# Optimization experiments

Measured on AMD Instinct MI355X. Metric: run time of the kernel, lower is better.

## Reference

```python
import jax, jax.numpy as jnp
import numpy as np

N = 50000      # nodes
E = 800000     # edges
HID = 64       # hidden_dim
HEADS = 4
DH = HID // HEADS
PIN = 128      # person_in_dim
DIN = 64       # disease_in_dim
NEXP = 4       # num_experts
K = 2          # topk
L = 2          # n_layers
NEG = 0.2      # gat_neg_slope


def setup_inputs() -> dict:
    key = jax.random.key(0)
    ks = iter(jax.random.split(key, 64))
    nrm = lambda shp, s=0.05: jax.random.normal(next(ks), shp, jnp.float32) * s
    d = {}
    d["features"] = jax.random.normal(next(ks), (N, PIN), jnp.float32)
    d["node_types"] = jax.random.randint(next(ks), (N,), 0, 2)
    d["src"] = jax.random.randint(next(ks), (E,), 0, N)
    d["dst"] = jax.random.randint(next(ks), (E,), 0, N)
    d["W_person"] = nrm((PIN, HID)); d["b_person"] = jnp.zeros((HID,), jnp.float32)
    d["W_disease"] = nrm((DIN, HID)); d["b_disease"] = jnp.zeros((HID,), jnp.float32)
    d["gat_W"] = nrm((L, HID, HID)); d["gat_al"] = nrm((L, HEADS, DH)); d["gat_ar"] = nrm((L, HEADS, DH))
    d["gin_eps"] = jnp.zeros((L,), jnp.float32)
    d["gin_W1"] = nrm((L, HID, HID)); d["gin_b1"] = jnp.zeros((L, HID), jnp.float32)
    d["gin_W2"] = nrm((L, HID, HID)); d["gin_b2"] = jnp.zeros((L, HID), jnp.float32)
    for p in ("gat", "gin"):
        d[p + "_gW"] = nrm((HID, NEXP)); d[p + "_gb"] = jnp.zeros((NEXP,), jnp.float32)
        d[p + "_eW1"] = nrm((NEXP, HID, HID // 2)); d[p + "_eb1"] = jnp.zeros((NEXP, HID // 2), jnp.float32)
        d[p + "_eW2"] = nrm((NEXP, HID // 2, HID)); d[p + "_eb2"] = jnp.zeros((NEXP, HID), jnp.float32)
    d["fg_W1"] = nrm((2 * HID, HID)); d["fg_b1"] = jnp.zeros((HID,), jnp.float32)
    d["fg_W2"] = nrm((HID, HID)); d["fg_b2"] = jnp.zeros((HID,), jnp.float32)
    return d


def _edge_softmax(logits, dst):
    m = jax.ops.segment_max(logits, dst, num_segments=N)
    e = jnp.exp(logits - m[dst])
    s = jax.ops.segment_sum(e, dst, num_segments=N)
    return e / (s[dst] + 1e-9)


def _gat(h, src, dst, gat_W, gat_al, gat_ar):
    for l in range(L):
        hW = (h @ gat_W[l]).reshape(N, HEADS, DH)
        el = (hW * gat_al[l]).sum(-1)                    # [N, HEADS]
        er = (hW * gat_ar[l]).sum(-1)
        lg = jax.nn.leaky_relu(el[src] + er[dst], NEG)   # [E, HEADS]
        a = _edge_softmax(lg, dst)
        out = jax.ops.segment_sum(hW[src] * a[:, :, None], dst, num_segments=N)
        h2 = out.reshape(N, HID) + h                     # residual=True
        h = jax.nn.relu(h2) if l < L - 1 else h2
    return h


def _gin(h, src, dst, gin_eps, gin_W1, gin_b1, gin_W2, gin_b2):
    deg = jax.ops.segment_sum(jnp.ones((E,), jnp.float32), dst, num_segments=N)
    inv = 1.0 / jnp.maximum(deg, 1.0)
    for l in range(L):
        agg = jax.ops.segment_sum(h[src], dst, num_segments=N) * inv[:, None]  # 'mean' aggregator
        x = (1.0 + gin_eps[l]) * h + agg                 # learn_eps=True
        x = jax.nn.relu(x @ gin_W1[l] + gin_b1[l]) @ gin_W2[l] + gin_b2[l]     # 2-layer MLP
        h = jax.nn.relu(x) if l < L - 1 else x
    return h


def _expert(h, gW, gb, eW1, eb1, eW2, eb2):
    probs = jax.nn.softmax(h @ gW + gb, axis=-1)         # [N, NEXP]
    topv, topi = jax.lax.top_k(probs, K)
    topv = topv / topv.sum(-1, keepdims=True)
    hot = jax.nn.one_hot(topi, NEXP, dtype=h.dtype)      # [N, K, NEXP]
    w = (hot * topv[..., None]).sum(1)                   # [N, NEXP] sparse weights
    e1 = jax.nn.relu(jnp.einsum('nd,edh->neh', h, eW1) + eb1)
    e2 = jnp.einsum('neh,ehd->ned', e1, eW2) + eb2       # [N, NEXP, HID]
    out = (e2 * w[:, :, None]).sum(1)
    f = hot.sum(1).mean(0)                               # routed fraction per expert
    P = probs.mean(0)
    aux = NEXP * jnp.sum(f * P)                          # switch-style load balancing
    return out, aux


def reference(features, node_types, src, dst, W_person, b_person, W_disease, b_disease,
              gat_W, gat_al, gat_ar, gin_eps, gin_W1, gin_b1, gin_W2, gin_b2,
              gat_gW, gat_gb, gat_eW1, gat_eb1, gat_eW2, gat_eb2,
              gin_gW, gin_gb, gin_eW1, gin_eb1, gin_eW2, gin_eb2,
              fg_W1, fg_b1, fg_W2, fg_b2):
    # per-type projection + scatter into shared buffer
    hp = features[:, :PIN] @ W_person + b_person
    hd = features[:, :DIN] @ W_disease + b_disease
    h = jnp.where((node_types == 0)[:, None], hp, hd)
    z_gat = _gat(h, src, dst, gat_W, gat_al, gat_ar)
    z_gin = _gin(h, src, dst, gin_eps, gin_W1, gin_b1, gin_W2, gin_b2)
    zg, aux_g = _expert(z_gat, gat_gW, gat_gb, gat_eW1, gat_eb1, gat_eW2, gat_eb2)
    zi, aux_i = _expert(z_gin, gin_gW, gin_gb, gin_eW1, gin_eb1, gin_eW2, gin_eb2)
    z = zi * zg
    u = jnp.concatenate([zg, zi], axis=-1)
    gate = jax.nn.sigmoid(jax.nn.relu(u @ fg_W1 + fg_b1) @ fg_W2 + fg_b2)
    u_prime = gate  # source calls fusion_gate(u) twice -> identical deterministic value
    z = gate * z + (1.0 - gate) * u_prime
    return z, aux_i + aux_g
```

## Files before the change

kernel.cpp:

```cpp
#include <hip/hip_runtime.h>

#define NN 50000
#define EE 800000
#define NEG 0.2f
#define NBG 391
#define NBT 392
#define NBKT 391
#define EPB 4096
#define NSEG 196

typedef __attribute__((ext_vector_type(8))) short s8;
typedef __attribute__((ext_vector_type(4))) float f4;

__device__ __forceinline__ float leaky(float x) { return x > 0.f ? x : NEG * x; }
__device__ __forceinline__ unsigned bf16r(float x) {
    unsigned u = __float_as_uint(x);
    return (u + 0x7fffu + ((u >> 16) & 1u)) >> 16;
}
__device__ __forceinline__ float lo16(unsigned p) { return __uint_as_float(p << 16); }
__device__ __forceinline__ float hi16(unsigned p) { return __uint_as_float(p & 0xffff0000u); }

__device__ __forceinline__ s8 a_from_f32(const float* p) {
    float4 u = *reinterpret_cast<const float4*>(p);
    float4 v = *reinterpret_cast<const float4*>(p + 4);
    s8 r;
    r[0] = (short)bf16r(u.x); r[1] = (short)bf16r(u.y);
    r[2] = (short)bf16r(u.z); r[3] = (short)bf16r(u.w);
    r[4] = (short)bf16r(v.x); r[5] = (short)bf16r(v.y);
    r[6] = (short)bf16r(v.z); r[7] = (short)bf16r(v.w);
    return r;
}

__global__ __launch_bounds__(256) void k_binA_pre(
        const int* __restrict__ src, const int* __restrict__ dst,
        int* __restrict__ seg_off, int* __restrict__ seg_cnt,
        unsigned* __restrict__ gseg, int* __restrict__ bucket_tot,
        const float* __restrict__ feat, const int* __restrict__ types,
        const float* __restrict__ Wp, const float* __restrict__ bp,
        const float* __restrict__ Wd, const float* __restrict__ bd,
        const float* __restrict__ gW, const float* __restrict__ al,
        const float* __restrict__ ar,
        float* __restrict__ h0f, unsigned* __restrict__ P,
        float* __restrict__ el, float* __restrict__ er) {
    __shared__ unsigned short WpT[64 * 136];
    __shared__ unsigned short WdT[64 * 72];
    __shared__ unsigned short WgT[64 * 72];
    __shared__ unsigned short y0s[4][16 * 72];
    if (blockIdx.x < NSEG) {
        unsigned* sbuf = (unsigned*)WpT;
        int* cnt = (int*)WdT;
        int* pre = (int*)WgT;
        int* ssc = (int*)y0s;
        for (int i = threadIdx.x; i < NBKT; i += 256) cnt[i] = 0;
        __syncthreads();
        int e0 = blockIdx.x * EPB;
        int nE = EE - e0; if (nE > EPB) nE = EPB;
        int b[16]; unsigned val[16]; int rk[16];
        #pragma unroll
        for (int i = 0; i < 16; i++) {
            int li = i * 256 + threadIdx.x;
            if (li < nE) {
                int e = e0 + li;
                int d = dst[e], s = src[e];
                b[i] = d >> 7;
                val[i] = ((unsigned)s << 7) | (unsigned)(d & 127);
                rk[i] = atomicAdd(&cnt[b[i]], 1);
            } else b[i] = -1;
        }
        __syncthreads();
        int t = threadIdx.x;
        int c0 = (2 * t     < NBKT) ? cnt[2 * t]     : 0;
        int c1 = (2 * t + 1 < NBKT) ? cnt[2 * t + 1] : 0;
        ssc[t] = c0 + c1;
        __syncthreads();
        for (int off = 1; off < 256; off <<= 1) {
            int u = (t >= off) ? ssc[t - off] : 0;
            __syncthreads();
            ssc[t] += u;
            __syncthreads();
        }
        int base = ssc[t] - (c0 + c1);
        pre[2 * t] = base;
        pre[2 * t + 1] = base + c0;
        __syncthreads();
        #pragma unroll
        for (int i = 0; i < 16; i++)
            if (b[i] >= 0) sbuf[pre[b[i]] + rk[i]] = val[i];
        for (int i = t; i < NBKT; i += 256) {
            seg_off[blockIdx.x * NBKT + i] = pre[i];
            seg_cnt[blockIdx.x * NBKT + i] = cnt[i];
            atomicAdd(&bucket_tot[i], cnt[i]);
        }
        __syncthreads();
        for (int i = t; i < nE; i += 256)
            gseg[(size_t)blockIdx.x * EPB + i] = sbuf[i];
        return;
    }
    for (int idx = threadIdx.x; idx < 128 * 64; idx += 256) {
        int k = idx >> 6, n = idx & 63;
        WpT[n * 136 + k] = (unsigned short)bf16r(Wp[idx]);
    }
    for (int idx = threadIdx.x; idx < 64 * 64; idx += 256) {
        int k = idx >> 6, n = idx & 63;
        WdT[n * 72 + k] = (unsigned short)bf16r(Wd[idx]);
        WgT[n * 72 + k] = (unsigned short)bf16r(gW[idx]);
    }
    __syncthreads();
    int wv = threadIdx.x >> 6, lane = threadIdx.x & 63;
    int quad = lane >> 4, l16 = lane & 15;
    int gw2 = (blockIdx.x - NSEG) * 4 + wv;
    int mtEnd = gw2 * 2 + 2; if (mtEnd > 3125) mtEnd = 3125;
    for (int mt = gw2 * 2; mt < mtEnd; mt++) {
        int row0 = mt * 16;
        const float* arow = feat + (size_t)(row0 + l16) * 128;
        f4 accp[4], accd[4];
        #pragma unroll
        for (int t = 0; t < 4; t++) { accp[t] = f4{0.f,0.f,0.f,0.f}; accd[t] = f4{0.f,0.f,0.f,0.f}; }
        #pragma unroll
        for (int ks = 0; ks < 4; ks++) {
            s8 a = a_from_f32(arow + ks * 32 + quad * 8);
            #pragma unroll
            for (int t = 0; t < 4; t++) {
                s8 b = *(const s8*)&WpT[(t * 16 + l16) * 136 + ks * 32 + quad * 8];
                accp[t] = __builtin_amdgcn_mfma_f32_16x16x32_bf16(a, b, accp[t], 0, 0, 0);
                if (ks < 2) {
                    s8 bd_ = *(const s8*)&WdT[(t * 16 + l16) * 72 + ks * 32 + quad * 8];
                    accd[t] = __builtin_amdgcn_mfma_f32_16x16x32_bf16(a, bd_, accd[t], 0, 0, 0);
                }
            }
        }
        int ty[4];
        #pragma unroll
        for (int r = 0; r < 4; r++) ty[r] = types[row0 + quad * 4 + r];
        float vv[4][4];
        #pragma unroll
        for (int t = 0; t < 4; t++) {
            int col = t * 16 + l16;
            float bpv = bp[col], bdv = bd[col];
            #pragma unroll
            for (int r = 0; r < 4; r++) {
                float v = ty[r] ? (accd[t][r] + bdv) : (accp[t][r] + bpv);
                vv[t][r] = v;
                h0f[(size_t)(row0 + quad * 4 + r) * 64 + col] = v;
                y0s[wv][(quad * 4 + r) * 72 + col] = (unsigned short)bf16r(v);
            }
        }
        s8 a0 = *(const s8*)&y0s[wv][l16 * 72 + quad * 8];
        s8 a1 = *(const s8*)&y0s[wv][l16 * 72 + 32 + quad * 8];
        f4 hw[4];
        #pragma unroll
        for (int t = 0; t < 4; t++) {
            hw[t] = f4{0.f,0.f,0.f,0.f};
            s8 b0 = *(const s8*)&WgT[(t * 16 + l16) * 72 + quad * 8];
            hw[t] = __builtin_amdgcn_mfma_f32_16x16x32_bf16(a0, b0, hw[t], 0, 0, 0);
            s8 b1_ = *(const s8*)&WgT[(t * 16 + l16) * 72 + 32 + quad * 8];
            hw[t] = __builtin_amdgcn_mfma_f32_16x16x32_bf16(a1, b1_, hw[t], 0, 0, 0);
        }
        #pragma unroll
        for (int t = 0; t < 4; t++) {
            int col = t * 16 + l16;
            float alv = al[col], arv = ar[col];
            #pragma unroll
            for (int r = 0; r < 4; r++) {
                int row = row0 + quad * 4 + r;
                float h = hw[t][r];
                P[(size_t)row * 64 + col] = bf16r(h) | (bf16r(vv[t][r]) << 16);
                float pl = h * alv, pr = h * arv;
                #pragma unroll
                for (int m = 1; m < 16; m <<= 1) {
                    pl += __shfl_xor(pl, m, 64);
                    pr += __shfl_xor(pr, m, 64);
                }
                if (l16 == 0) {
                    el[(size_t)row * 4 + t] = pl;
                    er[(size_t)row * 4 + t] = pr;
                }
            }
        }
    }
}

__global__ __launch_bounds__(256) void k_binB(
        int* __restrict__ row_start, const int* __restrict__ seg_off,
        const int* __restrict__ seg_cnt, const unsigned* __restrict__ gseg,
        int* __restrict__ csr_src, const int* __restrict__ bucket_tot) {
    __shared__ int spre[256];
    __shared__ int soff[NSEG];
    __shared__ int ss[256];
    __shared__ int kur[128];
    __shared__ int sred[4];
    int b = blockIdx.x;
    int t = threadIdx.x;
    int bt = 0;
    for (int i = t; i < b; i += 256) bt += bucket_tot[i];
    #pragma unroll
    for (int o2 = 1; o2 < 64; o2 <<= 1) bt += __shfl_xor(bt, o2, 64);
    if ((t & 63) == 0) sred[t >> 6] = bt;
    int c0 = (t < NSEG) ? seg_cnt[t * NBKT + b] : 0;
    if (t < NSEG) soff[t] = seg_off[t * NBKT + b];
    ss[t] = c0;
    __syncthreads();
    int bstart = sred[0] + sred[1] + sred[2] + sred[3];
    for (int off = 1; off < 256; off <<= 1) {
        int u = (t >= off) ? ss[t - off] : 0;
        __syncthreads();
        ss[t] += u;
        __syncthreads();
    }
    spre[t] = ss[t] - c0;
    int cntb = ss[255];
    if (t < 128) kur[t] = 0;
    __syncthreads();
    for (int idx = t; idx < cntb; idx += 256) {
        int lo = 0, hi = 255;
        #pragma unroll
        for (int s = 0; s < 8; s++) {
            int mid = (lo + hi + 1) >> 1;
            if (spre[mid] <= idx) lo = mid; else hi = mid - 1;
        }
        unsigned v = gseg[(size_t)lo * EPB + soff[lo] + (idx - spre[lo])];
        atomicAdd(&kur[v & 127], 1);
    }
    __syncthreads();
    int deg = (t < 128) ? kur[t] : 0;
    ss[t] = deg;
    __syncthreads();
    for (int off = 1; off < 256; off <<= 1) {
        int u = (t >= off) ? ss[t - off] : 0;
        __syncthreads();
        ss[t] += u;
        __syncthreads();
    }
    if (t < 128) {
        int cur = bstart + ss[t] - deg;
        kur[t] = cur;
        int d = (b << 7) + t;
        if (d < NN) row_start[d] = cur;
    }
    if (b == 0 && t == 0) row_start[NN] = EE;
    __syncthreads();
    for (int idx = t; idx < cntb; idx += 256) {
        int lo = 0, hi = 255;
        #pragma unroll
        for (int s = 0; s < 8; s++) {
            int mid = (lo + hi + 1) >> 1;
            if (spre[mid] <= idx) lo = mid; else hi = mid - 1;
        }
        unsigned v = gseg[(size_t)lo * EPB + soff[lo] + (idx - spre[lo])];
        int p = atomicAdd(&kur[v & 127], 1);
        csr_src[p] = (int)(v >> 7);
    }
}

template <int RELU>
__global__ void k_edges(const int* __restrict__ rows, const int* __restrict__ csr,
                        const unsigned* __restrict__ Pin,
                        const float* __restrict__ el, const float* __restrict__ er,
                        const float* __restrict__ gat_in, const float* __restrict__ gin_in,
                        const float* __restrict__ eps_p,
                        float* __restrict__ vgf, unsigned short* __restrict__ vgb,
                        unsigned short* __restrict__ xb) {
    __shared__ float ews[4][256];
    int wv = threadIdx.x >> 6, lane = threadIdx.x & 63;
    int n = blockIdx.x * 4 + wv;
    int st = rows[n], dg = rows[n + 1] - st;
    int hd = lane >> 4;
    float4 erv = *reinterpret_cast<const float4*>(er + (size_t)n * 4);
    float accg = 0.f, acci = 0.f, ssum = 0.f;
    for (int base = 0; base < dg; base += 64) {
        int rem = dg - base; if (rem > 64) rem = 64;
        int myi = 0;
        if (lane < rem) {
            myi = csr[st + base + lane];
            float4 lv = *reinterpret_cast<const float4*>(el + (size_t)myi * 4);
            float4 ev;
            ev.x = __expf(leaky(lv.x + erv.x));
            ev.y = __expf(leaky(lv.y + erv.y));
            ev.z = __expf(leaky(lv.z + erv.z));
            ev.w = __expf(leaky(lv.w + erv.w));
            *reinterpret_cast<float4*>(&ews[wv][lane * 4]) = ev;
        }
        int j = 0;
        for (; j + 4 <= rem; j += 4) {
            int s0 = __shfl(myi, j, 64),     s1 = __shfl(myi, j + 1, 64);
            int s2 = __shfl(myi, j + 2, 64), s3 = __shfl(myi, j + 3, 64);
            unsigned p0 = Pin[(size_t)s0 * 64 + lane];
            unsigned p1 = Pin[(size_t)s1 * 64 + lane];
            unsigned p2 = Pin[(size_t)s2 * 64 + lane];
            unsigned p3 = Pin[(size_t)s3 * 64 + lane];
            float a0 = ews[wv][(j + 0) * 4 + hd];
            float a1 = ews[wv][(j + 1) * 4 + hd];
            float a2 = ews[wv][(j + 2) * 4 + hd];
            float a3 = ews[wv][(j + 3) * 4 + hd];
            accg += a0 * lo16(p0) + a1 * lo16(p1) + a2 * lo16(p2) + a3 * lo16(p3);
            acci += hi16(p0) + hi16(p1) + hi16(p2) + hi16(p3);
            ssum += a0 + a1 + a2 + a3;
        }
        for (; j < rem; j++) {
            int s0 = __shfl(myi, j, 64);
            unsigned p0 = Pin[(size_t)s0 * 64 + lane];
            float a0 = ews[wv][j * 4 + hd];
            accg += a0 * lo16(p0); acci += hi16(p0); ssum += a0;
        }
    }
    float vg = accg / (ssum + 1e-9f) + gat_in[(size_t)n * 64 + lane];
    if (RELU) vg = fmaxf(vg, 0.f);
    float invd = 1.0f / fmaxf((float)dg, 1.0f);
    float x = (1.0f + eps_p[0]) * gin_in[(size_t)n * 64 + lane] + acci * invd;
    size_t off = (size_t)n * 64 + lane;
    vgf[off] = vg;
    vgb[off] = (unsigned short)bf16r(vg);
    xb[off] = (unsigned short)bf16r(x);
}

template <int L>
__global__ __launch_bounds__(256) void k_mlp(const unsigned short* __restrict__ Gx,
        const unsigned short* __restrict__ Eb,
        const float* __restrict__ W1, const float* __restrict__ b1,
        const float* __restrict__ W2, const float* __restrict__ b2,
        const float* __restrict__ gatW, const float* __restrict__ al,
        const float* __restrict__ ar,
        unsigned short* __restrict__ Fb, float* __restrict__ Cf,
        unsigned* __restrict__ P, float* __restrict__ el, float* __restrict__ er,
        const float* __restrict__ Zg, const float* __restrict__ ggW,
        const float* __restrict__ ggb, const float* __restrict__ igW,
        const float* __restrict__ igb,
        float* __restrict__ wgtg, float* __restrict__ wgti,
        float* __restrict__ stats) {
    __shared__ unsigned short W1T[64 * 72];
    __shared__ unsigned short W2T[64 * 72];
    __shared__ unsigned short WgT[(L == 0) ? 64 * 72 : 64];
    __shared__ unsigned short y1s[4][16 * 72];
    __shared__ float sstat[16];
    if (L == 1 && threadIdx.x < 16) sstat[threadIdx.x] = 0.f;
    for (int idx = threadIdx.x; idx < 64 * 64; idx += 256) {
        int k = idx >> 6, n = idx & 63;
        W1T[n * 72 + k] = (unsigned short)bf16r(W1[idx]);
        W2T[n * 72 + k] = (unsigned short)bf16r(W2[idx]);
        if (L == 0) WgT[n * 72 + k] = (unsigned short)bf16r(gatW[idx]);
    }
    __syncthreads();
    int wv = threadIdx.x >> 6, lane = threadIdx.x & 63;
    int quad = lane >> 4, l16 = lane & 15;
    int gw = blockIdx.x * 4 + wv;
    int mtEnd = gw * 2 + 2; if (mtEnd > 3125) mtEnd = 3125;
    float sp[2][4] = {{0,0,0,0},{0,0,0,0}};
    float sh[2][4] = {{0,0,0,0},{0,0,0,0}};
    for (int mt = gw * 2; mt < mtEnd; mt++) {
        int row0 = mt * 16;
        const unsigned short* arow = Gx + (size_t)(row0 + l16) * 64;
        s8 a0 = *(const s8*)(arow + quad * 8);
        s8 a1 = *(const s8*)(arow + 32 + quad * 8);
        f4 acc1[4];
        #pragma unroll
        for (int t = 0; t < 4; t++) {
            acc1[t] = f4{0.f,0.f,0.f,0.f};
            s8 b0 = *(const s8*)&W1T[(t * 16 + l16) * 72 + quad * 8];
            acc1[t] = __builtin_amdgcn_mfma_f32_16x16x32_bf16(a0, b0, acc1[t], 0, 0, 0);
            s8 b1_ = *(const s8*)&W1T[(t * 16 + l16) * 72 + 32 + quad * 8];
            acc1[t] = __builtin_amdgcn_mfma_f32_16x16x32_bf16(a1, b1_, acc1[t], 0, 0, 0);
        }
        #pragma unroll
        for (int t = 0; t < 4; t++) {
            float b1v = b1[t * 16 + l16];
            #pragma unroll
            for (int r = 0; r < 4; r++) {
                float v = fmaxf(acc1[t][r] + b1v, 0.f);
                y1s[wv][(quad * 4 + r) * 72 + t * 16 + l16] = (unsigned short)bf16r(v);
            }
        }
        s8 c0 = *(const s8*)&y1s[wv][l16 * 72 + quad * 8];
        s8 c1 = *(const s8*)&y1s[wv][l16 * 72 + 32 + quad * 8];
        f4 acc2[4];
        #pragma unroll
        for (int t = 0; t < 4; t++) {
            acc2[t] = f4{0.f,0.f,0.f,0.f};
            s8 b0 = *(const s8*)&W2T[(t * 16 + l16) * 72 + quad * 8];
            acc2[t] = __builtin_amdgcn_mfma_f32_16x16x32_bf16(c0, b0, acc2[t], 0, 0, 0);
            s8 b1_ = *(const s8*)&W2T[(t * 16 + l16) * 72 + 32 + quad * 8];
            acc2[t] = __builtin_amdgcn_mfma_f32_16x16x32_bf16(c1, b1_, acc2[t], 0, 0, 0);
        }
        unsigned short vb[4][4];
        float vout[4][4];
        #pragma unroll
        for (int t = 0; t < 4; t++) {
            int col = t * 16 + l16;
            float b2v = b2[col];
            #pragma unroll
            for (int r = 0; r < 4; r++) {
                float v = acc2[t][r] + b2v;
                if (L == 0) v = fmaxf(v, 0.f);
                size_t off = (size_t)(row0 + quad * 4 + r) * 64 + col;
                unsigned short vb16 = (unsigned short)bf16r(v);
                vb[t][r] = vb16;
                vout[t][r] = v;
                Fb[off] = vb16;
                if (L == 0) Cf[off] = v;
            }
        }
        if (L == 0) {
            const unsigned short* erow = Eb + (size_t)(row0 + l16) * 64;
            s8 e0 = *(const s8*)(erow + quad * 8);
            s8 e1 = *(const s8*)(erow + 32 + quad * 8);
            f4 hw[4];
            #pragma unroll
            for (int t = 0; t < 4; t++) {
                hw[t] = f4{0.f,0.f,0.f,0.f};
                s8 b0 = *(const s8*)&WgT[(t * 16 + l16) * 72 + quad * 8];
                hw[t] = __builtin_amdgcn_mfma_f32_16x16x32_bf16(e0, b0, hw[t], 0, 0, 0);
                s8 b1_ = *(const s8*)&WgT[(t * 16 + l16) * 72 + 32 + quad * 8];
                hw[t] = __builtin_amdgcn_mfma_f32_16x16x32_bf16(e1, b1_, hw[t], 0, 0, 0);
            }
            #pragma unroll
            for (int t = 0; t < 4; t++) {
                int col = t * 16 + l16;
                float alv = al[col], arv = ar[col];
                #pragma unroll
                for (int r = 0; r < 4; r++) {
                    int row = row0 + quad * 4 + r;
                    float h = hw[t][r];
                    P[(size_t)row * 64 + col] = bf16r(h) | ((unsigned)vb[t][r] << 16);
                    float pl = h * alv, pr = h * arv;
                    #pragma unroll
                    for (int m = 1; m < 16; m <<= 1) {
                        pl += __shfl_xor(pl, m, 64);
                        pr += __shfl_xor(pr, m, 64);
                    }
                    if (l16 == 0) {
                        el[(size_t)row * 4 + t] = pl;
                        er[(size_t)row * 4 + t] = pr;
                    }
                }
            }
        } else {
            #pragma unroll
            for (int r = 0; r < 4; r++) {
                int row = row0 + quad * 4 + r;
                float pg[4] = {0,0,0,0}, pi[4] = {0,0,0,0};
                #pragma unroll
                for (int t = 0; t < 4; t++) {
                    int col = t * 16 + l16;
                    float zgv = Zg[(size_t)row * 64 + col];
                    float ziv = vout[t][r];
                    #pragma unroll
                    for (int e = 0; e < 4; e++) {
                        pg[e] += zgv * ggW[col * 4 + e];
                        pi[e] += ziv * igW[col * 4 + e];
                    }
                }
                #pragma unroll
                for (int m = 1; m < 16; m <<= 1) {
                    #pragma unroll
                    for (int e = 0; e < 4; e++) {
                        pg[e] += __shfl_xor(pg[e], m, 64);
                        pi[e] += __shfl_xor(pi[e], m, 64);
                    }
                }
                if (l16 == 0) {
                    #pragma unroll
                    for (int q = 0; q < 2; q++) {
                        float lg0 = (q ? pi[0] + igb[0] : pg[0] + ggb[0]);
                        float lg1 = (q ? pi[1] + igb[1] : pg[1] + ggb[1]);
                        float lg2 = (q ? pi[2] + igb[2] : pg[2] + ggb[2]);
                        float lg3 = (q ? pi[3] + igb[3] : pg[3] + ggb[3]);
                        float mx = fmaxf(fmaxf(lg0, lg1), fmaxf(lg2, lg3));
                        float ex0 = __expf(lg0 - mx), ex1 = __expf(lg1 - mx);
                        float ex2 = __expf(lg2 - mx), ex3 = __expf(lg3 - mx);
                        float inv = 1.0f / (ex0 + ex1 + ex2 + ex3);
                        float pr4[4] = {ex0 * inv, ex1 * inv, ex2 * inv, ex3 * inv};
                        int i1 = 0; float v1 = pr4[0];
                        #pragma unroll
                        for (int t = 1; t < 4; t++) if (pr4[t] > v1) { v1 = pr4[t]; i1 = t; }
                        int i2 = -1; float v2 = -1.f;
                        #pragma unroll
                        for (int t = 0; t < 4; t++) if (t != i1 && pr4[t] > v2) { v2 = pr4[t]; i2 = t; }
                        float wsum = v1 + v2;
                        float wq[4] = {0.f, 0.f, 0.f, 0.f};
                        wq[i1] = v1 / wsum; wq[i2] = v2 / wsum;
                        float* WD = q ? wgti : wgtg;
                        *reinterpret_cast<float4*>(WD + (size_t)row * 4) =
                            float4{wq[0], wq[1], wq[2], wq[3]};
                        #pragma unroll
                        for (int t = 0; t < 4; t++) sp[q][t] += pr4[t];
                        sh[q][i1] += 1.f; sh[q][i2] += 1.f;
                    }
                }
            }
        }
    }
    if (L == 1) {
        __syncthreads();
        if (l16 == 0) {
            #pragma unroll
            for (int q = 0; q < 2; q++)
                #pragma unroll
                for (int e = 0; e < 4; e++) {
                    atomicAdd(&sstat[q * 8 + e], sp[q][e]);
                    atomicAdd(&sstat[q * 8 + 4 + e], sh[q][e]);
                }
        }
        __syncthreads();
        if (threadIdx.x < 16) atomicAdd(&stats[threadIdx.x], sstat[threadIdx.x]);
    }
}

__global__ __launch_bounds__(256) void k_tail(const unsigned short* __restrict__ Eb,
        const unsigned short* __restrict__ Fb,
        const float* __restrict__ g_eW1, const float* __restrict__ g_eb1,
        const float* __restrict__ g_eW2, const float* __restrict__ g_eb2,
        const float* __restrict__ i_eW1, const float* __restrict__ i_eb1,
        const float* __restrict__ i_eW2, const float* __restrict__ i_eb2,
        const float* __restrict__ wgtg, const float* __restrict__ wgti,
        const float* __restrict__ W1, const float* __restrict__ b1,
        const float* __restrict__ W2, const float* __restrict__ b2,
        unsigned short* __restrict__ ub, float* __restrict__ out,
        const float* __restrict__ stats) {
    __shared__ unsigned short wbuf[4 * 32 * 72 + 4 * 64 * 40];
    __shared__ unsigned short y1s[4][16 * 72];
    int wv = threadIdx.x >> 6, lane = threadIdx.x & 63;
    int quad = lane >> 4, l16 = lane & 15;
    int gw = blockIdx.x * 4 + wv;
    int mt0 = gw * 2;
    f4 moe[2][2][4];
    #pragma unroll
    for (int p = 0; p < 2; p++)
        #pragma unroll
        for (int m = 0; m < 2; m++)
            #pragma unroll
            for (int t = 0; t < 4; t++) moe[p][m][t] = f4{0.f,0.f,0.f,0.f};
    #pragma unroll
    for (int p = 0; p < 2; p++) {
        const unsigned short* Ab = p ? Fb : Eb;
        const float* eW1 = p ? i_eW1 : g_eW1;
        const float* eb1 = p ? i_eb1 : g_eb1;
        const float* eW2 = p ? i_eW2 : g_eW2;
        const float* eb2 = p ? i_eb2 : g_eb2;
        const float* wgt = p ? wgti : wgtg;
        int qoff = p ? 64 : 0;
        if (p) __syncthreads();
        for (int g = threadIdx.x; g < 8192; g += 256) {
            int e = g >> 11, rem = g & 2047;
            int k = rem >> 5, n = rem & 31;
            wbuf[e * 2304 + n * 72 + k] = (unsigned short)bf16r(eW1[g]);
        }
        for (int g = threadIdx.x; g < 8192; g += 256) {
            int e = g >> 11, rem = g & 2047;
            int k = rem >> 6, n = rem & 63;
            wbuf[9216 + e * 2560 + n * 40 + k] = (unsigned short)bf16r(eW2[g]);
        }
        __syncthreads();
        #pragma unroll
        for (int m = 0; m < 2; m++) {
            int mt = mt0 + m;
            if (mt < 3125) {
                int row0 = mt * 16;
                const unsigned short* arow = Ab + (size_t)(row0 + l16) * 64;
                s8 a0 = *(const s8*)(arow + quad * 8);
                s8 a1 = *(const s8*)(arow + 32 + quad * 8);
                for (int e = 0; e < 4; e++) {
                    f4 acc1[2];
                    #pragma unroll
                    for (int t = 0; t < 2; t++) {
                        acc1[t] = f4{0.f,0.f,0.f,0.f};
                        s8 b0 = *(const s8*)&wbuf[e * 2304 + (t * 16 + l16) * 72 + quad * 8];
                        acc1[t] = __builtin_amdgcn_mfma_f32_16x16x32_bf16(a0, b0, acc1[t], 0, 0, 0);
                        s8 b1_ = *(const s8*)&wbuf[e * 2304 + (t * 16 + l16) * 72 + 32 + quad * 8];
                        acc1[t] = __builtin_amdgcn_mfma_f32_16x16x32_bf16(a1, b1_, acc1[t], 0, 0, 0);
                    }
                    #pragma unroll
                    for (int t = 0; t < 2; t++) {
                        float b1v = eb1[e * 32 + t * 16 + l16];
                        #pragma unroll
                        for (int r = 0; r < 4; r++) {
                            float v = fmaxf(acc1[t][r] + b1v, 0.f);
                            y1s[wv][(quad * 4 + r) * 40 + t * 16 + l16] = (unsigned short)bf16r(v);
                        }
                    }
                    s8 a2 = *(const s8*)&y1s[wv][l16 * 40 + quad * 8];
                    f4 acc2[4];
                    #pragma unroll
                    for (int t = 0; t < 4; t++) {
                        acc2[t] = f4{0.f,0.f,0.f,0.f};
                        s8 b2_ = *(const s8*)&wbuf[9216 + e * 2560 + (t * 16 + l16) * 40 + quad * 8];
                        acc2[t] = __builtin_amdgcn_mfma_f32_16x16x32_bf16(a2, b2_, acc2[t], 0, 0, 0);
                    }
                    #pragma unroll
                    for (int t = 0; t < 4; t++) {
                        float b2v = eb2[e * 64 + t * 16 + l16];
                        #pragma unroll
                        for (int r = 0; r < 4; r++) {
                            float we = wgt[(size_t)(row0 + quad * 4 + r) * 4 + e];
                            moe[p][m][t][r] += we * (acc2[t][r] + b2v);
                        }
                    }
                }
                #pragma unroll
                for (int t = 0; t < 4; t++) {
                    int col = t * 16 + l16;
                    #pragma unroll
                    for (int r = 0; r < 4; r++) {
                        int row = row0 + quad * 4 + r;
                        ub[(size_t)row * 128 + qoff + col] = (unsigned short)bf16r(moe[p][m][t][r]);
                    }
                }
            }
        }
    }
    __syncthreads();
    for (int idx = threadIdx.x; idx < 128 * 64; idx += 256) {
        int k = idx >> 6, n = idx & 63;
        wbuf[n * 136 + k] = (unsigned short)bf16r(W1[idx]);
    }
    for (int idx = threadIdx.x; idx < 64 * 64; idx += 256) {
        int k = idx >> 6, n = idx & 63;
        wbuf[8704 + n * 72 + k] = (unsigned short)bf16r(W2[idx]);
    }
    __syncthreads();
    #pragma unroll
    for (int m = 0; m < 2; m++) {
        int mt = mt0 + m;
        if (mt < 3125) {
            int row0 = mt * 16;
            const unsigned short* arow = ub + (size_t)(row0 + l16) * 128;
            f4 acc1[4];
            #pragma unroll
            for (int t = 0; t < 4; t++) acc1[t] = f4{0.f,0.f,0.f,0.f};
            #pragma unroll
            for (int ks = 0; ks < 4; ks++) {
                s8 a = *(const s8*)(arow + ks * 32 + quad * 8);
                #pragma unroll
                for (int t = 0; t < 4; t++) {
                    s8 b = *(const s8*)&wbuf[(t * 16 + l16) * 136 + ks * 32 + quad * 8];
                    acc1[t] = __builtin_amdgcn_mfma_f32_16x16x32_bf16(a, b, acc1[t], 0, 0, 0);
                }
            }
            #pragma unroll
            for (int t = 0; t < 4; t++) {
                float b1v = b1[t * 16 + l16];
                #pragma unroll
                for (int r = 0; r < 4; r++) {
                    float v = fmaxf(acc1[t][r] + b1v, 0.f);
                    y1s[wv][(quad * 4 + r) * 72 + t * 16 + l16] = (unsigned short)bf16r(v);
                }
            }
            f4 acc2[4];
            #pragma unroll
            for (int t = 0; t < 4; t++) acc2[t] = f4{0.f,0.f,0.f,0.f};
            #pragma unroll
            for (int ks = 0; ks < 2; ks++) {
                s8 a = *(const s8*)&y1s[wv][l16 * 72 + ks * 32 + quad * 8];
                #pragma unroll
                for (int t = 0; t < 4; t++) {
                    s8 b = *(const s8*)&wbuf[8704 + (t * 16 + l16) * 72 + ks * 32 + quad * 8];
                    acc2[t] = __builtin_amdgcn_mfma_f32_16x16x32_bf16(a, b, acc2[t], 0, 0, 0);
                }
            }
            #pragma unroll
            for (int t = 0; t < 4; t++) {
                int col = t * 16 + l16;
                float b2v = b2[col];
                #pragma unroll
                for (int r = 0; r < 4; r++) {
                    int row = row0 + quad * 4 + r;
                    float g = 1.0f / (1.0f + __expf(-(acc2[t][r] + b2v)));
                    float zgv = moe[0][m][t][r];
                    float ziv = moe[1][m][t][r];
                    out[(size_t)row * 64 + col] = g * zgv * ziv + (1.0f - g) * g;
                }
            }
        }
    }
    if (blockIdx.x == 0 && threadIdx.x < 64) {
        int t = threadIdx.x;
        float s = (t < 16) ? stats[t] : 0.f;
        float aux = 0.f;
        for (int q = 0; q < 2; q++) {
            float a = 0.f;
            for (int e = 0; e < 4; e++) {
                float pr = __shfl(s, q * 8 + e, 64);
                float f  = __shfl(s, q * 8 + 4 + e, 64);
                a += (f / (float)NN) * (pr / (float)NN);
            }
            aux += 4.0f * a;
        }
        if (t == 0) out[(size_t)NN * 64] = aux;
    }
}

extern "C" void kernel_launch(void* const* d_in, const int* in_sizes, int n_in,
                              void* d_out, int out_size, void* d_ws, size_t ws_size,
                              hipStream_t stream) {
    (void)in_sizes; (void)n_in; (void)out_size; (void)ws_size;
    const float* features  = (const float*)d_in[0];
    const int*   node_types= (const int*)d_in[1];
    const int*   src       = (const int*)d_in[2];
    const int*   dst       = (const int*)d_in[3];
    const float* W_person  = (const float*)d_in[4];
    const float* b_person  = (const float*)d_in[5];
    const float* W_disease = (const float*)d_in[6];
    const float* b_disease = (const float*)d_in[7];
    const float* gat_W     = (const float*)d_in[8];
    const float* gat_al    = (const float*)d_in[9];
    const float* gat_ar    = (const float*)d_in[10];
    const float* gin_eps   = (const float*)d_in[11];
    const float* gin_W1    = (const float*)d_in[12];
    const float* gin_b1    = (const float*)d_in[13];
    const float* gin_W2    = (const float*)d_in[14];
    const float* gin_b2    = (const float*)d_in[15];
    const float* gat_gW    = (const float*)d_in[16];
    const float* gat_gb    = (const float*)d_in[17];
    const float* gat_eW1   = (const float*)d_in[18];
    const float* gat_eb1   = (const float*)d_in[19];
    const float* gat_eW2   = (const float*)d_in[20];
    const float* gat_eb2   = (const float*)d_in[21];
    const float* gin_gW    = (const float*)d_in[22];
    const float* gin_gb    = (const float*)d_in[23];
    const float* gin_eW1   = (const float*)d_in[24];
    const float* gin_eb1   = (const float*)d_in[25];
    const float* gin_eW2   = (const float*)d_in[26];
    const float* gin_eb2   = (const float*)d_in[27];
    const float* fg_W1     = (const float*)d_in[28];
    const float* fg_b1     = (const float*)d_in[29];
    const float* fg_W2     = (const float*)d_in[30];
    const float* fg_b2     = (const float*)d_in[31];
    float* out = (float*)d_out;

    float* ws = (float*)d_ws;
    size_t o = 0;
    float* A = ws + o; o += (size_t)NN * 64;
    float* B = ws + o; o += (size_t)NN * 64;
    float* C = ws + o; o += (size_t)NN * 64;
    unsigned short* E  = (unsigned short*)(ws + o); o += (size_t)NN * 32;
    unsigned short* F  = (unsigned short*)(ws + o); o += (size_t)NN * 32;
    unsigned short* G  = (unsigned short*)(ws + o); o += (size_t)NN * 32;
    unsigned* P = (unsigned*)(ws + o); o += (size_t)NN * 64;
    float* el = ws + o; o += (size_t)NN * 4;
    float* er = ws + o; o += (size_t)NN * 4;
    float* wgtg = ws + o; o += (size_t)NN * 4;
    float* wgti = ws + o; o += (size_t)NN * 4;
    int* bucket_tot = (int*)(ws + o); o += 392;
    float* stats    = ws + o; o += 16;
    int* row_start = (int*)(ws + o); o += NN + 4;
    int* csr_src   = (int*)(ws + o); o += EE;
    int* seg_off   = (int*)(ws + o); o += NSEG * NBKT + 64;
    int* seg_cnt   = (int*)(ws + o); o += NSEG * NBKT + 64;
    unsigned* gseg = (unsigned*)(ws + o); o += (size_t)NSEG * EPB;

    unsigned short* ub = (unsigned short*)A;

    const int NB_node = NN / 4;

    hipMemsetAsync(bucket_tot, 0, sizeof(int) * 392 + sizeof(float) * 16, stream);

    k_binA_pre<<<NSEG + NBG, 256, 0, stream>>>(src, dst, seg_off, seg_cnt, gseg, bucket_tot,
                                               features, node_types, W_person, b_person,
                                               W_disease, b_disease, gat_W, gat_al, gat_ar,
                                               A, P, el, er);

    k_binB<<<NBKT, 256, 0, stream>>>(row_start, seg_off, seg_cnt, gseg, csr_src, bucket_tot);

    k_edges<1><<<NB_node, 256, 0, stream>>>(row_start, csr_src, P, el, er, A, A,
                                            gin_eps, B, E, G);
    k_mlp<0><<<NBG, 256, 0, stream>>>(G, E, gin_W1, gin_b1, gin_W2, gin_b2,
                                      gat_W + 4096, gat_al + 64, gat_ar + 64,
                                      F, C, P, el, er,
                                      nullptr, nullptr, nullptr, nullptr, nullptr,
                                      nullptr, nullptr, nullptr);

    k_edges<0><<<NB_node, 256, 0, stream>>>(row_start, csr_src, P, el, er, B, C,
                                            gin_eps + 1, B, E, G);
    k_mlp<1><<<NBG, 256, 0, stream>>>(G, nullptr, gin_W1 + 4096, gin_b1 + 64,
                                      gin_W2 + 4096, gin_b2 + 64,
                                      nullptr, nullptr, nullptr,
                                      F, nullptr, nullptr, nullptr, nullptr,
                                      B, gat_gW, gat_gb, gin_gW, gin_gb,
                                      wgtg, wgti, stats);

    k_tail<<<NBT, 256, 0, stream>>>(E, F,
                                    gat_eW1, gat_eb1, gat_eW2, gat_eb2,
                                    gin_eW1, gin_eb1, gin_eW2, gin_eb2,
                                    wgtg, wgti, fg_W1, fg_b1, fg_W2, fg_b2,
                                    ub, out, stats);
}
```

Baseline: 316.4 us.

## Fuse edge aggregation into per-layer MLP kernel with LDS staging

Merges the per-node edge-gather kernel and the GIN MLP / next-layer GAT projection kernel into one k_layer kernel. Each wave aggregates 16 nodes, stages the bf16 GIN input and GAT output in LDS, and then runs the MFMA MLP directly on them, so the G/E/Zg intermediates are no longer written to and reread from global memory. The P/el/er buffers are double-buffered so layer 0 can write the next layer's projections while other blocks still read the current ones. The trade-off is less parallelism in the gather phase: one wave now walks 16 nodes serially with only 782 blocks, and LDS use per block grows, which may lower occupancy.

```diff
diff --git a/kernel.cpp b/kernel.cpp
--- a/kernel.cpp
+++ b/kernel.cpp
@@ -4,6 +4,7 @@
 #define EE 800000
 #define NEG 0.2f
 #define NBG 391
+#define NBL 782
 #define NBT 392
 #define NBKT 391
 #define EPB 4096
@@ -252,85 +253,30 @@
     }
 }
 
-template <int RELU>
-__global__ void k_edges(const int* __restrict__ rows, const int* __restrict__ csr,
-                        const unsigned* __restrict__ Pin,
-                        const float* __restrict__ el, const float* __restrict__ er,
-                        const float* __restrict__ gat_in, const float* __restrict__ gin_in,
-                        const float* __restrict__ eps_p,
-                        float* __restrict__ vgf, unsigned short* __restrict__ vgb,
-                        unsigned short* __restrict__ xb) {
-    __shared__ float ews[4][256];
-    int wv = threadIdx.x >> 6, lane = threadIdx.x & 63;
-    int n = blockIdx.x * 4 + wv;
-    int st = rows[n], dg = rows[n + 1] - st;
-    int hd = lane >> 4;
-    float4 erv = *reinterpret_cast<const float4*>(er + (size_t)n * 4);
-    float accg = 0.f, acci = 0.f, ssum = 0.f;
-    for (int base = 0; base < dg; base += 64) {
-        int rem = dg - base; if (rem > 64) rem = 64;
-        int myi = 0;
-        if (lane < rem) {
-            myi = csr[st + base + lane];
-            float4 lv = *reinterpret_cast<const float4*>(el + (size_t)myi * 4);
-            float4 ev;
-            ev.x = __expf(leaky(lv.x + erv.x));
-            ev.y = __expf(leaky(lv.y + erv.y));
-            ev.z = __expf(leaky(lv.z + erv.z));
-            ev.w = __expf(leaky(lv.w + erv.w));
-            *reinterpret_cast<float4*>(&ews[wv][lane * 4]) = ev;
-        }
-        int j = 0;
-        for (; j + 4 <= rem; j += 4) {
-            int s0 = __shfl(myi, j, 64),     s1 = __shfl(myi, j + 1, 64);
-            int s2 = __shfl(myi, j + 2, 64), s3 = __shfl(myi, j + 3, 64);
-            unsigned p0 = Pin[(size_t)s0 * 64 + lane];
-            unsigned p1 = Pin[(size_t)s1 * 64 + lane];
-            unsigned p2 = Pin[(size_t)s2 * 64 + lane];
-            unsigned p3 = Pin[(size_t)s3 * 64 + lane];
-            float a0 = ews[wv][(j + 0) * 4 + hd];
-            float a1 = ews[wv][(j + 1) * 4 + hd];
-            float a2 = ews[wv][(j + 2) * 4 + hd];
-            float a3 = ews[wv][(j + 3) * 4 + hd];
-            accg += a0 * lo16(p0) + a1 * lo16(p1) + a2 * lo16(p2) + a3 * lo16(p3);
-            acci += hi16(p0) + hi16(p1) + hi16(p2) + hi16(p3);
-            ssum += a0 + a1 + a2 + a3;
-        }
-        for (; j < rem; j++) {
-            int s0 = __shfl(myi, j, 64);
-            unsigned p0 = Pin[(size_t)s0 * 64 + lane];
-            float a0 = ews[wv][j * 4 + hd];
-            accg += a0 * lo16(p0); acci += hi16(p0); ssum += a0;
-        }
-    }
-    float vg = accg / (ssum + 1e-9f) + gat_in[(size_t)n * 64 + lane];
-    if (RELU) vg = fmaxf(vg, 0.f);
-    float invd = 1.0f / fmaxf((float)dg, 1.0f);
-    float x = (1.0f + eps_p[0]) * gin_in[(size_t)n * 64 + lane] + acci * invd;
-    size_t off = (size_t)n * 64 + lane;
-    vgf[off] = vg;
-    vgb[off] = (unsigned short)bf16r(vg);
-    xb[off] = (unsigned short)bf16r(x);
-}
-
 template <int L>
-__global__ __launch_bounds__(256) void k_mlp(const unsigned short* __restrict__ Gx,
-        const unsigned short* __restrict__ Eb,
+__global__ __launch_bounds__(256) void k_layer(
+        const int* __restrict__ rows, const int* __restrict__ csr,
+        const unsigned* __restrict__ Pin,
+        const float* __restrict__ eli, const float* __restrict__ eri,
+        const float* __restrict__ gat_in, const float* __restrict__ gin_in,
+        const float* __restrict__ eps_p,
         const float* __restrict__ W1, const float* __restrict__ b1,
         const float* __restrict__ W2, const float* __restrict__ b2,
         const float* __restrict__ gatW, const float* __restrict__ al,
         const float* __restrict__ ar,
+        float* __restrict__ vgf, unsigned short* __restrict__ vgb,
         unsigned short* __restrict__ Fb, float* __restrict__ Cf,
-        unsigned* __restrict__ P, float* __restrict__ el, float* __restrict__ er,
-        const float* __restrict__ Zg, const float* __restrict__ ggW,
-        const float* __restrict__ ggb, const float* __restrict__ igW,
-        const float* __restrict__ igb,
+        unsigned* __restrict__ Po, float* __restrict__ elo, float* __restrict__ ero,
+        const float* __restrict__ ggW, const float* __restrict__ ggb,
+        const float* __restrict__ igW, const float* __restrict__ igb,
         float* __restrict__ wgtg, float* __restrict__ wgti,
         float* __restrict__ stats) {
     __shared__ unsigned short W1T[64 * 72];
     __shared__ unsigned short W2T[64 * 72];
     __shared__ unsigned short WgT[(L == 0) ? 64 * 72 : 64];
-    __shared__ unsigned short y1s[4][16 * 72];
+    __shared__ unsigned short S[4][(L == 0) ? 2304 : 1152];
+    __shared__ float zs[(L == 1) ? 4096 : 4];
+    __shared__ float ews[4][256];
     __shared__ float sstat[16];
     if (L == 1 && threadIdx.x < 16) sstat[threadIdx.x] = 0.f;
     for (int idx = threadIdx.x; idx < 64 * 64; idx += 256) {
@@ -342,15 +288,70 @@
     __syncthreads();
     int wv = threadIdx.x >> 6, lane = threadIdx.x & 63;
     int quad = lane >> 4, l16 = lane & 15;
-    int gw = blockIdx.x * 4 + wv;
-    int mtEnd = gw * 2 + 2; if (mtEnd > 3125) mtEnd = 3125;
+    int mt = blockIdx.x * 4 + wv;
+    float eps0 = eps_p[0];
     float sp[2][4] = {{0,0,0,0},{0,0,0,0}};
     float sh[2][4] = {{0,0,0,0},{0,0,0,0}};
-    for (int mt = gw * 2; mt < mtEnd; mt++) {
+    if (mt < 3125) {
         int row0 = mt * 16;
-        const unsigned short* arow = Gx + (size_t)(row0 + l16) * 64;
-        s8 a0 = *(const s8*)(arow + quad * 8);
-        s8 a1 = *(const s8*)(arow + 32 + quad * 8);
+        for (int j = 0; j < 16; j++) {
+            int n = row0 + j;
+            int st = rows[n], dg = rows[n + 1] - st;
+            float4 erv = *reinterpret_cast<const float4*>(eri + (size_t)n * 4);
+            float accg = 0.f, acci = 0.f, ssum = 0.f;
+            for (int base = 0; base < dg; base += 64) {
+                int rem = dg - base; if (rem > 64) rem = 64;
+                int myi = 0;
+                if (lane < rem) {
+                    myi = csr[st + base + lane];
+                    float4 lv = *reinterpret_cast<const float4*>(eli + (size_t)myi * 4);
+                    float4 ev;
+                    ev.x = __expf(leaky(lv.x + erv.x));
+                    ev.y = __expf(leaky(lv.y + erv.y));
+                    ev.z = __expf(leaky(lv.z + erv.z));
+                    ev.w = __expf(leaky(lv.w + erv.w));
+                    *reinterpret_cast<float4*>(&ews[wv][lane * 4]) = ev;
+                }
+                int jj = 0;
+                for (; jj + 4 <= rem; jj += 4) {
+                    int s0 = __shfl(myi, jj, 64),     s1 = __shfl(myi, jj + 1, 64);
+                    int s2 = __shfl(myi, jj + 2, 64), s3 = __shfl(myi, jj + 3, 64);
+                    unsigned p0 = Pin[(size_t)s0 * 64 + lane];
+                    unsigned p1 = Pin[(size_t)s1 * 64 + lane];
+                    unsigned p2 = Pin[(size_t)s2 * 64 + lane];
+                    unsigned p3 = Pin[(size_t)s3 * 64 + lane];
+                    float a0 = ews[wv][(jj + 0) * 4 + quad];
+                    float a1 = ews[wv][(jj + 1) * 4 + quad];
+                    float a2 = ews[wv][(jj + 2) * 4 + quad];
+                    float a3 = ews[wv][(jj + 3) * 4 + quad];
+                    accg += a0 * lo16(p0) + a1 * lo16(p1) + a2 * lo16(p2) + a3 * lo16(p3);
+                    acci += hi16(p0) + hi16(p1) + hi16(p2) + hi16(p3);
+                    ssum += a0 + a1 + a2 + a3;
+                }
+                for (; jj < rem; jj++) {
+                    int s0 = __shfl(myi, jj, 64);
+                    unsigned p0 = Pin[(size_t)s0 * 64 + lane];
+                    float a0 = ews[wv][jj * 4 + quad];
+                    accg += a0 * lo16(p0); acci += hi16(p0); ssum += a0;
+                }
+            }
+            float vg = accg / (ssum + 1e-9f) + gat_in[(size_t)n * 64 + lane];
+            if (L == 0) vg = fmaxf(vg, 0.f);
+            float invd = 1.0f / fmaxf((float)dg, 1.0f);
+            float x = (1.0f + eps0) * gin_in[(size_t)n * 64 + lane] + acci * invd;
+            if (L == 0) vgf[(size_t)n * 64 + lane] = vg;
+            if (L == 1) vgb[(size_t)n * 64 + lane] = (unsigned short)bf16r(vg);
+            S[wv][j * 72 + lane] = (unsigned short)bf16r(x);
+            if (L == 0) S[wv][1152 + j * 72 + lane] = (unsigned short)bf16r(vg);
+            if (L == 1) zs[wv * 1024 + j * 64 + lane] = vg;
+        }
+        s8 a0 = *(const s8*)&S[wv][l16 * 72 + quad * 8];
+        s8 a1 = *(const s8*)&S[wv][l16 * 72 + 32 + quad * 8];
+        s8 e0{}, e1{};
+        if (L == 0) {
+            e0 = *(const s8*)&S[wv][1152 + l16 * 72 + quad * 8];
+            e1 = *(const s8*)&S[wv][1152 + l16 * 72 + 32 + quad * 8];
+        }
         f4 acc1[4];
         #pragma unroll
         for (int t = 0; t < 4; t++) {
@@ -366,11 +367,11 @@
             #pragma unroll
             for (int r = 0; r < 4; r++) {
                 float v = fmaxf(acc1[t][r] + b1v, 0.f);
-                y1s[wv][(quad * 4 + r) * 72 + t * 16 + l16] = (unsigned short)bf16r(v);
-            }
-        }
-        s8 c0 = *(const s8*)&y1s[wv][l16 * 72 + quad * 8];
-        s8 c1 = *(const s8*)&y1s[wv][l16 * 72 + 32 + quad * 8];
+                S[wv][(quad * 4 + r) * 72 + t * 16 + l16] = (unsigned short)bf16r(v);
+            }
+        }
+        s8 c0 = *(const s8*)&S[wv][l16 * 72 + quad * 8];
+        s8 c1 = *(const s8*)&S[wv][l16 * 72 + 32 + quad * 8];
         f4 acc2[4];
         #pragma unroll
         for (int t = 0; t < 4; t++) {
@@ -390,7 +391,7 @@
             for (int r = 0; r < 4; r++) {
                 float v = acc2[t][r] + b2v;
                 if (L == 0) v = fmaxf(v, 0.f);
-                size_t off = (size_t)(row0 + quad * 4 + r) * 64 + col;
+                size_t off = (size_t)(mt * 16 + quad * 4 + r) * 64 + col;
                 unsigned short vb16 = (unsigned short)bf16r(v);
                 vb[t][r] = vb16;
                 vout[t][r] = v;
@@ -399,9 +400,6 @@
             }
         }
         if (L == 0) {
-            const unsigned short* erow = Eb + (size_t)(row0 + l16) * 64;
-            s8 e0 = *(const s8*)(erow + quad * 8);
-            s8 e1 = *(const s8*)(erow + 32 + quad * 8);
             f4 hw[4];
             #pragma unroll
             for (int t = 0; t < 4; t++) {
@@ -419,7 +417,7 @@
                 for (int r = 0; r < 4; r++) {
                     int row = row0 + quad * 4 + r;
                     float h = hw[t][r];
-                    P[(size_t)row * 64 + col] = bf16r(h) | ((unsigned)vb[t][r] << 16);
+                    Po[(size_t)row * 64 + col] = bf16r(h) | ((unsigned)vb[t][r] << 16);
                     float pl = h * alv, pr = h * arv;
                     #pragma unroll
                     for (int m = 1; m < 16; m <<= 1) {
@@ -427,8 +425,8 @@
                         pr += __shfl_xor(pr, m, 64);
                     }
                     if (l16 == 0) {
-                        el[(size_t)row * 4 + t] = pl;
-                        er[(size_t)row * 4 + t] = pr;
+                        elo[(size_t)row * 4 + t] = pl;
+                        ero[(size_t)row * 4 + t] = pr;
                     }
                 }
             }
@@ -440,7 +438,7 @@
                 #pragma unroll
                 for (int t = 0; t < 4; t++) {
                     int col = t * 16 + l16;
-                    float zgv = Zg[(size_t)row * 64 + col];
+                    float zgv = zs[wv * 1024 + (quad * 4 + r) * 64 + col];
                     float ziv = vout[t][r];
                     #pragma unroll
                     for (int e = 0; e < 4; e++) {
@@ -732,10 +730,12 @@
     float* C = ws + o; o += (size_t)NN * 64;
     unsigned short* E  = (unsigned short*)(ws + o); o += (size_t)NN * 32;
     unsigned short* F  = (unsigned short*)(ws + o); o += (size_t)NN * 32;
-    unsigned short* G  = (unsigned short*)(ws + o); o += (size_t)NN * 32;
-    unsigned* P = (unsigned*)(ws + o); o += (size_t)NN * 64;
-    float* el = ws + o; o += (size_t)NN * 4;
-    float* er = ws + o; o += (size_t)NN * 4;
+    unsigned* P0 = (unsigned*)(ws + o); o += (size_t)NN * 64;
+    unsigned* P1 = (unsigned*)(ws + o); o += (size_t)NN * 64;
+    float* el0 = ws + o; o += (size_t)NN * 4;
+    float* er0 = ws + o; o += (size_t)NN * 4;
+    float* el1 = ws + o; o += (size_t)NN * 4;
+    float* er1 = ws + o; o += (size_t)NN * 4;
     float* wgtg = ws + o; o += (size_t)NN * 4;
     float* wgti = ws + o; o += (size_t)NN * 4;
     int* bucket_tot = (int*)(ws + o); o += 392;
@@ -748,33 +748,28 @@
 
     unsigned short* ub = (unsigned short*)A;
 
-    const int NB_node = NN / 4;
-
     hipMemsetAsync(bucket_tot, 0, sizeof(int) * 392 + sizeof(float) * 16, stream);
 
     k_binA_pre<<<NSEG + NBG, 256, 0, stream>>>(src, dst, seg_off, seg_cnt, gseg, bucket_tot,
                                                features, node_types, W_person, b_person,
                                                W_disease, b_disease, gat_W, gat_al, gat_ar,
-                                               A, P, el, er);
+                                               A, P0, el0, er0);
 
     k_binB<<<NBKT, 256, 0, stream>>>(row_start, seg_off, seg_cnt, gseg, csr_src, bucket_tot);
 
-    k_edges<1><<<NB_node, 256, 0, stream>>>(row_start, csr_src, P, el, er, A, A,
-                                            gin_eps, B, E, G);
-    k_mlp<0><<<NBG, 256, 0, stream>>>(G, E, gin_W1, gin_b1, gin_W2, gin_b2,
-                                      gat_W + 4096, gat_al + 64, gat_ar + 64,
-                                      F, C, P, el, er,
-                                      nullptr, nullptr, nullptr, nullptr, nullptr,
-                                      nullptr, nullptr, nullptr);
-
-    k_edges<0><<<NB_node, 256, 0, stream>>>(row_start, csr_src, P, el, er, B, C,
-                                            gin_eps + 1, B, E, G);
-    k_mlp<1><<<NBG, 256, 0, stream>>>(G, nullptr, gin_W1 + 4096, gin_b1 + 64,
-                                      gin_W2 + 4096, gin_b2 + 64,
-                                      nullptr, nullptr, nullptr,
-                                      F, nullptr, nullptr, nullptr, nullptr,
-                                      B, gat_gW, gat_gb, gin_gW, gin_gb,
-                                      wgtg, wgti, stats);
+    k_layer<0><<<NBL, 256, 0, stream>>>(row_start, csr_src, P0, el0, er0, A, A, gin_eps,
+                                        gin_W1, gin_b1, gin_W2, gin_b2,
+                                        gat_W + 4096, gat_al + 64, gat_ar + 64,
+                                        B, E, F, C, P1, el1, er1,
+                                        nullptr, nullptr, nullptr, nullptr,
+                                        nullptr, nullptr, nullptr);
+
+    k_layer<1><<<NBL, 256, 0, stream>>>(row_start, csr_src, P1, el1, er1, B, C, gin_eps + 1,
+                                        gin_W1 + 4096, gin_b1 + 64, gin_W2 + 4096, gin_b2 + 64,
+                                        nullptr, nullptr, nullptr,
+                                        B, E, F, nullptr, nullptr, nullptr, nullptr,
+                                        gat_gW, gat_gb, gin_gW, gin_gb,
+                                        wgtg, wgti, stats);
 
     k_tail<<<NBT, 256, 0, stream>>>(E, F,
                                     gat_eW1, gat_eb1, gat_eW2, gat_eb2,
```

Result: slower. 457.3 us (+44.6%).
